# Kernel optimization log

Measured on AMD Instinct MI355X. Metric: run time of the kernel, lower is better.

Reference implementation:

```python
import jax, jax.numpy as jnp
import numpy as np

N_EXPERTS = 8
D_IN = 2048
D_OUT = 2048
BATCH = 8192


def setup_inputs() -> dict:
    key = jax.random.key(0)
    k_x, k_w, k_b, k_a, k_m = jax.random.split(key, 5)
    xs = jax.random.normal(k_x, (BATCH, D_IN), dtype=jnp.float32)
    # Expert parameters: each submodule modeled as Linear(D_IN, D_OUT)
    W = jax.random.normal(k_w, (N_EXPERTS, D_IN, D_OUT), dtype=jnp.float32) / np.sqrt(D_IN)
    b = jax.random.normal(k_b, (N_EXPERTS, D_OUT), dtype=jnp.float32) * 0.01
    actions = jax.random.randint(k_a, (BATCH,), 0, N_EXPERTS, dtype=jnp.int32)
    mxs = jax.random.randint(k_m, (BATCH,), 0, N_EXPERTS, dtype=jnp.int32)  # pass-through metadata
    return {"xs": xs, "W": W, "b": b, "mxs": mxs, "actions": actions}


def reference(xs, W, b, mxs, actions):
    # Original: per-sample split, route sample i to submodule actions[i], concat.
    # Vectorized MoE dispatch-combine: compute all expert outputs, select by one-hot.
    onehot = jax.nn.one_hot(actions, W.shape[0], dtype=xs.dtype)  # [B, E]
    # y_all[b,e,f] = xs[b,:] @ W[e,:,:]; combine with one-hot selection, add routed bias.
    ys = jnp.einsum('be,bd,edf->bf', onehot, xs, W) + b[actions]  # [B, D_OUT]
    return (ys, mxs, actions)
```

## Files before the change

kernel.cpp:

```cpp
#include <hip/hip_runtime.h>
#include <hip/hip_bf16.h>
#include <stdint.h>

#define BATCH 8192
#define BATCH_PAD (BATCH + 128)
#define DIN   2048
#define DOUT  2048
#define NEXP  8
#define BM    128
#define BN    256
#define BK    64
#define NT    (DIN / BK)
#define ASZ   16384
#define TSZ   49152

typedef __attribute__((ext_vector_type(4))) float fx4;
typedef __attribute__((ext_vector_type(8))) short sx8;

__device__ __forceinline__ short f2b(float x){
  unsigned u = __float_as_uint(x);
  u = u + 0x7FFFu + ((u >> 16) & 1u);
  return (short)(u >> 16);
}

__device__ __forceinline__ void gload16(const void* g, void* l){
  __builtin_amdgcn_global_load_lds(
      (const __attribute__((address_space(1))) unsigned int*)g,
      (__attribute__((address_space(3))) unsigned int*)l, 16, 0, 0);
}

__global__ void prep_kernel(const int* __restrict__ actions, const int* __restrict__ mxs,
                            int* __restrict__ perm, int* __restrict__ cnt_off,
                            float* __restrict__ out){
  __shared__ int cnt[NEXP], off[NEXP], cur[NEXP];
  int t = threadIdx.x;
  if (t < NEXP) cnt[t] = 0;
  __syncthreads();
  for (int i = t; i < BATCH; i += 256){
    atomicAdd(&cnt[actions[i]], 1);
    out[(size_t)BATCH * DOUT + i]         = (float)mxs[i];
    out[(size_t)BATCH * DOUT + BATCH + i] = (float)actions[i];
  }
  __syncthreads();
  if (t == 0){ int s = 0; for (int e = 0; e < NEXP; ++e){ off[e] = s; cur[e] = s; s += cnt[e]; } }
  __syncthreads();
  for (int i = t; i < BATCH; i += 256){
    int e = actions[i];
    int p = atomicAdd(&cur[e], 1);
    perm[p] = i;
  }
  if (t < NEXP){ cnt_off[t] = cnt[t]; cnt_off[NEXP + t] = off[t]; }
}

__global__ void gatherx_kernel(const float* __restrict__ xs, const int* __restrict__ perm,
                               short* __restrict__ xp){
  int i = blockIdx.x;
  int t = threadIdx.x;
  short v[8];
  if (i < BATCH){
    const fx4* src = (const fx4*)(xs + (size_t)perm[i] * DIN + t * 8);
    fx4 a = src[0], b2 = src[1];
    v[0]=f2b(a.x); v[1]=f2b(a.y); v[2]=f2b(a.z); v[3]=f2b(a.w);
    v[4]=f2b(b2.x); v[5]=f2b(b2.y); v[6]=f2b(b2.z); v[7]=f2b(b2.w);
  } else {
#pragma unroll
    for (int j = 0; j < 8; ++j) v[j] = 0;
  }
  *(sx8*)(xp + (size_t)i * DIN + t * 8) = *(const sx8*)v;
}

__global__ void transw_kernel(const float* __restrict__ W, short* __restrict__ Wt){
  __shared__ float tile[64][69];
  int e  = blockIdx.z;
  int n0 = blockIdx.x * 64;
  int k0 = blockIdx.y * 64;
  const float* Wp = W + (size_t)e * DIN * DOUT + (size_t)k0 * DOUT + n0;
  int t = threadIdx.x;
#pragma unroll
  for (int it = 0; it < 4; ++it){
    int r = it * 16 + (t >> 4);
    int c = (t & 15) * 4;
    fx4 v = *(const fx4*)(Wp + (size_t)r * DOUT + c);
    tile[r][c] = v.x; tile[r][c+1] = v.y; tile[r][c+2] = v.z; tile[r][c+3] = v.w;
  }
  __syncthreads();
  int n  = t >> 2;
  int kc = (t & 3) * 16;
  short vv[16];
#pragma unroll
  for (int j = 0; j < 16; ++j) vv[j] = f2b(tile[kc + j][n]);
  short* dst = Wt + (size_t)e * DOUT * DIN + (size_t)(n0 + n) * DIN + k0 + kc;
  *(sx8*)dst       = *(const sx8*)vv;
  *(sx8*)(dst + 8) = *(const sx8*)(vv + 8);
}

__global__ __launch_bounds__(512, 2)
void moe_gemm_kernel(const short* __restrict__ xp, const short* __restrict__ Wt,
                     const float* __restrict__ bias, const int* __restrict__ perm,
                     const int* __restrict__ cnt_off, float* __restrict__ out){
  extern __shared__ char lds[];

  int F    = blockIdx.x;
  int J    = (F & 7) * 512 + (F >> 3);
  int g    = J >> 6;
  int slot = J & 63;
  int e    = g >> 3;
  int nb   = g & 7;
  int cnt_e = cnt_off[e];
  if (slot * BM >= cnt_e) return;
  int off_e  = cnt_off[NEXP + e];
  int m_base = off_e + slot * BM;
  int m_cnt  = min(BM, cnt_e - slot * BM);
  int n0     = nb * BN;

  int t    = threadIdx.x;
  int wid  = t >> 6;
  int l    = t & 63;
  int wm   = wid & 1;
  int wn   = wid >> 1;
  int lrow = l & 15;
  int lk   = l >> 4;

  int csrc = (((t & 7) ^ ((t >> 3) & 7)) << 4);
  const char* agp[2];
  const char* bgp[4];
  {
    const char* xpB = (const char*)xp;
    const char* wtB = (const char*)Wt + (size_t)e * ((size_t)DOUT * DIN * 2);
#pragma unroll
    for (int j = 0; j < 2; ++j){
      int r = j * 64 + (t >> 3);
      agp[j] = xpB + (size_t)(m_base + r) * (DIN * 2) + csrc;
    }
#pragma unroll
    for (int j = 0; j < 4; ++j){
      int r = j * 64 + (t >> 3);
      bgp[j] = wtB + (size_t)(n0 + r) * (DIN * 2) + csrc;
    }
  }
  int da0 = t * 16,        da1 = 8192  + t * 16;
  int db0 = ASZ + t * 16,  db1 = ASZ + 8192 + t * 16;
  int db2 = ASZ + 16384 + t * 16, db3 = ASZ + 24576 + t * 16;

#define STG1(kt, base) do{ gload16(agp[0] + (size_t)(kt)*128, lds + (base) + da0); \
                           gload16(agp[1] + (size_t)(kt)*128, lds + (base) + da1); \
                           gload16(bgp[0] + (size_t)(kt)*128, lds + (base) + db0);}while(0)
#define STG2(kt, base) do{ gload16(bgp[1] + (size_t)(kt)*128, lds + (base) + db1); \
                           gload16(bgp[2] + (size_t)(kt)*128, lds + (base) + db2); \
                           gload16(bgp[3] + (size_t)(kt)*128, lds + (base) + db3);}while(0)

  int sw = (lrow & 7) << 4;
  int aoff[2][4], boff[2][4];
#pragma unroll
  for (int kk = 0; kk < 2; ++kk){
#pragma unroll
    for (int m = 0; m < 4; ++m)
      aoff[kk][m] = (wm * 64 + m * 16 + lrow) * 128 + (((kk * 4 + lk) * 16) ^ sw);
#pragma unroll
    for (int n = 0; n < 4; ++n)
      boff[kk][n] = ASZ + (wn * 64 + n * 16 + lrow) * 128 + (((kk * 4 + lk) * 16) ^ sw);
  }

  fx4 acc[4][4];
#pragma unroll
  for (int m = 0; m < 4; ++m)
#pragma unroll
    for (int n = 0; n < 4; ++n)
      acc[m][n] = (fx4){0.f, 0.f, 0.f, 0.f};

  float bcol[4];
#pragma unroll
  for (int n = 0; n < 4; ++n)
    bcol[n] = bias[(size_t)e * DOUT + n0 + wn * 64 + n * 16 + lrow];

  STG1(0, 0);     STG2(0, 0);
  STG1(1, TSZ);   STG2(1, TSZ);
  asm volatile("s_waitcnt vmcnt(6)" ::: "memory");
  __builtin_amdgcn_s_barrier();
  asm volatile("" ::: "memory");

  sx8 a0[4], a1[4], b0[4], b1[4];
#pragma unroll
  for (int m = 0; m < 4; ++m) a0[m] = *(const sx8*)(lds + aoff[0][m]);
#pragma unroll
  for (int n = 0; n < 4; ++n) b0[n] = *(const sx8*)(lds + boff[0][n]);

  int cmp = 0, nxt = TSZ, stg = 2 * TSZ;

  for (int kt = 0; kt < NT; ++kt){
#pragma unroll
    for (int m = 0; m < 4; ++m) a1[m] = *(const sx8*)(lds + cmp + aoff[1][m]);
#pragma unroll
    for (int n = 0; n < 4; ++n) b1[n] = *(const sx8*)(lds + cmp + boff[1][n]);
    if (kt + 2 < NT) STG1(kt + 2, stg);
    __builtin_amdgcn_s_setprio(1);
#pragma unroll
    for (int m = 0; m < 4; ++m)
#pragma unroll
      for (int n = 0; n < 4; ++n)
        acc[m][n] = __builtin_amdgcn_mfma_f32_16x16x32_bf16(a0[m], b0[n], acc[m][n], 0, 0, 0);
    __builtin_amdgcn_s_setprio(0);
    __builtin_amdgcn_s_barrier();
    asm volatile("" ::: "memory");

    if (kt + 2 < NT){
      STG2(kt + 2, stg);
      asm volatile("s_waitcnt vmcnt(6)" ::: "memory");
    } else {
      asm volatile("s_waitcnt vmcnt(0)" ::: "memory");
    }
    __builtin_amdgcn_s_barrier();
    asm volatile("" ::: "memory");
    if (kt + 1 < NT){
#pragma unroll
      for (int m = 0; m < 4; ++m) a0[m] = *(const sx8*)(lds + nxt + aoff[0][m]);
#pragma unroll
      for (int n = 0; n < 4; ++n) b0[n] = *(const sx8*)(lds + nxt + boff[0][n]);
    }
    __builtin_amdgcn_s_setprio(1);
#pragma unroll
    for (int m = 0; m < 4; ++m)
#pragma unroll
      for (int n = 0; n < 4; ++n)
        acc[m][n] = __builtin_amdgcn_mfma_f32_16x16x32_bf16(a1[m], b1[n], acc[m][n], 0, 0, 0);
    __builtin_amdgcn_s_setprio(0);
    __builtin_amdgcn_s_barrier();
    asm volatile("" ::: "memory");

    int tmp = cmp; cmp = nxt; nxt = stg; stg = tmp;
  }

#pragma unroll
  for (int m = 0; m < 4; ++m){
    int rb = wm * 64 + m * 16 + lk * 4;
    int prow[4];
#pragma unroll
    for (int q = 0; q < 4; ++q)
      prow[q] = (rb + q < m_cnt) ? perm[m_base + rb + q] : -1;
#pragma unroll
    for (int n = 0; n < 4; ++n){
      int col = n0 + wn * 64 + n * 16 + lrow;
      fx4 v = acc[m][n];
#pragma unroll
      for (int q = 0; q < 4; ++q)
        if (prow[q] >= 0)
          out[(size_t)prow[q] * DOUT + col] = v[q] + bcol[n];
    }
  }
#undef STG1
#undef STG2
}

extern "C" void kernel_launch(void* const* d_in, const int* in_sizes, int n_in,
                              void* d_out, int out_size, void* d_ws, size_t ws_size,
                              hipStream_t stream) {
  const float* xs      = (const float*)d_in[0];
  const float* W       = (const float*)d_in[1];
  const float* b       = (const float*)d_in[2];
  const int*   mxs     = (const int*)d_in[3];
  const int*   actions = (const int*)d_in[4];
  float* out = (float*)d_out;

  int*   perm    = (int*)d_ws;
  int*   cnt_off = perm + BATCH;
  short* Wt      = (short*)((char*)d_ws + 65536);
  short* xp      = (short*)((char*)d_ws + 65536 + (size_t)NEXP * DIN * DOUT * 2);

  hipLaunchKernelGGL(prep_kernel, dim3(1), dim3(256), 0, stream, actions, mxs, perm, cnt_off, out);
  hipLaunchKernelGGL(gatherx_kernel, dim3(BATCH_PAD), dim3(256), 0, stream, xs, perm, xp);
  hipLaunchKernelGGL(transw_kernel, dim3(DOUT/64, DIN/64, NEXP), dim3(256), 0, stream, W, Wt);
  hipLaunchKernelGGL(moe_gemm_kernel, dim3(64 * 64), dim3(512), 147456, stream,
                     xp, Wt, b, perm, cnt_off, out);
}
```

Baseline: 187.5 us.

## Pad expert groups to tile multiples, compact grid, halve BK with triple-buffered LDS

Expert row groups are now padded to multiples of 128 in the permutation, and a compact slot-to-expert table replaces the sparse 4096-block grid with about 576 blocks. The GEMM K tile drops from 64 to 32, giving a triple-buffered 72KB static LDS footprint and launch bounds raised to four blocks per CU. It also uses a new swizzled LDS layout and a single-phase k-step. This removes empty-block launch overhead and aims for higher occupancy, at the cost of more barriers per K and some padded rows computed on zeros.

```diff
diff --git a/kernel.cpp b/kernel.cpp
--- a/kernel.cpp
+++ b/kernel.cpp
@@ -3,16 +3,17 @@
 #include <stdint.h>
 
 #define BATCH 8192
-#define BATCH_PAD (BATCH + 128)
+#define GROWS 9216
 #define DIN   2048
 #define DOUT  2048
 #define NEXP  8
 #define BM    128
 #define BN    256
-#define BK    64
+#define BK    32
 #define NT    (DIN / BK)
-#define ASZ   16384
-#define TSZ   49152
+#define NSLOT 72
+#define BUFSZ 24576
+#define BOFF  8192
 
 typedef __attribute__((ext_vector_type(4))) float fx4;
 typedef __attribute__((ext_vector_type(8))) short sx8;
@@ -30,10 +31,11 @@
 }
 
 __global__ void prep_kernel(const int* __restrict__ actions, const int* __restrict__ mxs,
-                            int* __restrict__ perm, int* __restrict__ cnt_off,
+                            int* __restrict__ perm, int* __restrict__ meta,
                             float* __restrict__ out){
-  __shared__ int cnt[NEXP], off[NEXP], cur[NEXP];
+  __shared__ int cnt[NEXP], cur[NEXP];
   int t = threadIdx.x;
+  for (int i = t; i < GROWS; i += 256) perm[i] = -1;
   if (t < NEXP) cnt[t] = 0;
   __syncthreads();
   for (int i = t; i < BATCH; i += 256){
@@ -42,14 +44,21 @@
     out[(size_t)BATCH * DOUT + BATCH + i] = (float)actions[i];
   }
   __syncthreads();
-  if (t == 0){ int s = 0; for (int e = 0; e < NEXP; ++e){ off[e] = s; cur[e] = s; s += cnt[e]; } }
+  if (t == 0){
+    int s = 0, slot = 0;
+    for (int e = 0; e < NEXP; ++e){
+      cur[e] = s;
+      int ns = (cnt[e] + BM - 1) / BM;
+      for (int q = 0; q < ns; ++q) meta[17 + slot++] = e;
+      s += ns * BM;
+    }
+    meta[16] = slot;
+  }
   __syncthreads();
   for (int i = t; i < BATCH; i += 256){
     int e = actions[i];
-    int p = atomicAdd(&cur[e], 1);
-    perm[p] = i;
-  }
-  if (t < NEXP){ cnt_off[t] = cnt[t]; cnt_off[NEXP + t] = off[t]; }
+    perm[atomicAdd(&cur[e], 1)] = i;
+  }
 }
 
 __global__ void gatherx_kernel(const float* __restrict__ xs, const int* __restrict__ perm,
@@ -57,8 +66,9 @@
   int i = blockIdx.x;
   int t = threadIdx.x;
   short v[8];
-  if (i < BATCH){
-    const fx4* src = (const fx4*)(xs + (size_t)perm[i] * DIN + t * 8);
+  int p = perm[i];
+  if (p >= 0){
+    const fx4* src = (const fx4*)(xs + (size_t)p * DIN + t * 8);
     fx4 a = src[0], b2 = src[1];
     v[0]=f2b(a.x); v[1]=f2b(a.y); v[2]=f2b(a.z); v[3]=f2b(a.w);
     v[4]=f2b(b2.x); v[5]=f2b(b2.y); v[6]=f2b(b2.z); v[7]=f2b(b2.w);
@@ -94,23 +104,18 @@
   *(sx8*)(dst + 8) = *(const sx8*)(vv + 8);
 }
 
-__global__ __launch_bounds__(512, 2)
+__global__ __launch_bounds__(512, 4)
 void moe_gemm_kernel(const short* __restrict__ xp, const short* __restrict__ Wt,
                      const float* __restrict__ bias, const int* __restrict__ perm,
-                     const int* __restrict__ cnt_off, float* __restrict__ out){
-  extern __shared__ char lds[];
-
-  int F    = blockIdx.x;
-  int J    = (F & 7) * 512 + (F >> 3);
-  int g    = J >> 6;
-  int slot = J & 63;
-  int e    = g >> 3;
-  int nb   = g & 7;
-  int cnt_e = cnt_off[e];
-  if (slot * BM >= cnt_e) return;
-  int off_e  = cnt_off[NEXP + e];
-  int m_base = off_e + slot * BM;
-  int m_cnt  = min(BM, cnt_e - slot * BM);
+                     const int* __restrict__ meta, float* __restrict__ out){
+  __shared__ char lds[3 * BUFSZ];
+
+  int F = blockIdx.x;
+  int slot = F >> 3, nb = F & 7;
+  int nslots = meta[16];
+  if (slot >= nslots) return;
+  int e      = meta[17 + slot];
+  int m_base = slot * BM;
   int n0     = nb * BN;
 
   int t    = threadIdx.x;
@@ -121,45 +126,25 @@
   int lrow = l & 15;
   int lk   = l >> 4;
 
-  int csrc = (((t & 7) ^ ((t >> 3) & 7)) << 4);
-  const char* agp[2];
-  const char* bgp[4];
-  {
-    const char* xpB = (const char*)xp;
-    const char* wtB = (const char*)Wt + (size_t)e * ((size_t)DOUT * DIN * 2);
-#pragma unroll
-    for (int j = 0; j < 2; ++j){
-      int r = j * 64 + (t >> 3);
-      agp[j] = xpB + (size_t)(m_base + r) * (DIN * 2) + csrc;
-    }
-#pragma unroll
-    for (int j = 0; j < 4; ++j){
-      int r = j * 64 + (t >> 3);
-      bgp[j] = wtB + (size_t)(n0 + r) * (DIN * 2) + csrc;
-    }
-  }
-  int da0 = t * 16,        da1 = 8192  + t * 16;
-  int db0 = ASZ + t * 16,  db1 = ASZ + 8192 + t * 16;
-  int db2 = ASZ + 16384 + t * 16, db3 = ASZ + 24576 + t * 16;
-
-#define STG1(kt, base) do{ gload16(agp[0] + (size_t)(kt)*128, lds + (base) + da0); \
-                           gload16(agp[1] + (size_t)(kt)*128, lds + (base) + da1); \
-                           gload16(bgp[0] + (size_t)(kt)*128, lds + (base) + db0);}while(0)
-#define STG2(kt, base) do{ gload16(bgp[1] + (size_t)(kt)*128, lds + (base) + db1); \
-                           gload16(bgp[2] + (size_t)(kt)*128, lds + (base) + db2); \
-                           gload16(bgp[3] + (size_t)(kt)*128, lds + (base) + db3);}while(0)
-
-  int sw = (lrow & 7) << 4;
-  int aoff[2][4], boff[2][4];
-#pragma unroll
-  for (int kk = 0; kk < 2; ++kk){
-#pragma unroll
-    for (int m = 0; m < 4; ++m)
-      aoff[kk][m] = (wm * 64 + m * 16 + lrow) * 128 + (((kk * 4 + lk) * 16) ^ sw);
-#pragma unroll
-    for (int n = 0; n < 4; ++n)
-      boff[kk][n] = ASZ + (wn * 64 + n * 16 + lrow) * 128 + (((kk * 4 + lk) * 16) ^ sw);
-  }
+  int srow = ((t >> 3) << 1) | ((t >> 2) & 1);
+  int schk = (t & 3) ^ ((t >> 3) & 3);
+  const char* ag  = (const char*)xp + ((size_t)(m_base + srow) * DIN + schk * 8) * 2;
+  const char* bg0 = (const char*)Wt + (((size_t)e * DOUT + n0 + srow) * DIN + schk * 8) * 2;
+  const char* bg1 = bg0 + (size_t)128 * DIN * 2;
+  int ldst = t * 16;
+
+#define STAGE(kt, BASE) do{ \
+    gload16(ag  + (size_t)(kt) * 64, lds + (BASE) + ldst); \
+    gload16(bg0 + (size_t)(kt) * 64, lds + (BASE) + BOFF + ldst); \
+    gload16(bg1 + (size_t)(kt) * 64, lds + (BASE) + BOFF + 8192 + ldst); \
+  }while(0)
+
+  int arow = wm * 64 + lrow;
+  int aline = arow >> 1;
+  int addrA = aline * 128 + (arow & 1) * 64 + ((lk ^ (aline & 3)) << 4);
+  int brow = wn * 64 + lrow;
+  int bline = brow >> 1;
+  int addrB = BOFF + bline * 128 + (brow & 1) * 64 + ((lk ^ (bline & 3)) << 4);
 
   fx4 acc[4][4];
 #pragma unroll
@@ -173,62 +158,39 @@
   for (int n = 0; n < 4; ++n)
     bcol[n] = bias[(size_t)e * DOUT + n0 + wn * 64 + n * 16 + lrow];
 
-  STG1(0, 0);     STG2(0, 0);
-  STG1(1, TSZ);   STG2(1, TSZ);
-  asm volatile("s_waitcnt vmcnt(6)" ::: "memory");
+#define KSTEP(CB, SB, DOSTG, kt) do{ \
+    sx8 af[4], bf[4]; \
+    _Pragma("unroll") for (int m = 0; m < 4; ++m) \
+      af[m] = *(const sx8*)(lds + (CB) + addrA + m * 1024); \
+    _Pragma("unroll") for (int n = 0; n < 4; ++n) \
+      bf[n] = *(const sx8*)(lds + (CB) + addrB + n * 1024); \
+    if (DOSTG) STAGE((kt) + 2, SB); \
+    __builtin_amdgcn_s_setprio(1); \
+    _Pragma("unroll") for (int m = 0; m < 4; ++m) \
+    _Pragma("unroll") for (int n = 0; n < 4; ++n) \
+      acc[m][n] = __builtin_amdgcn_mfma_f32_16x16x32_bf16(af[m], bf[n], acc[m][n], 0, 0, 0); \
+    __builtin_amdgcn_s_setprio(0); \
+    if (DOSTG) asm volatile("s_waitcnt vmcnt(3)" ::: "memory"); \
+    else       asm volatile("s_waitcnt vmcnt(0)" ::: "memory"); \
+    __builtin_amdgcn_s_barrier(); \
+    asm volatile("" ::: "memory"); \
+  }while(0)
+
+  STAGE(0, 0);
+  STAGE(1, BUFSZ);
+  asm volatile("s_waitcnt vmcnt(3)" ::: "memory");
   __builtin_amdgcn_s_barrier();
   asm volatile("" ::: "memory");
 
-  sx8 a0[4], a1[4], b0[4], b1[4];
-#pragma unroll
-  for (int m = 0; m < 4; ++m) a0[m] = *(const sx8*)(lds + aoff[0][m]);
-#pragma unroll
-  for (int n = 0; n < 4; ++n) b0[n] = *(const sx8*)(lds + boff[0][n]);
-
-  int cmp = 0, nxt = TSZ, stg = 2 * TSZ;
-
-  for (int kt = 0; kt < NT; ++kt){
-#pragma unroll
-    for (int m = 0; m < 4; ++m) a1[m] = *(const sx8*)(lds + cmp + aoff[1][m]);
-#pragma unroll
-    for (int n = 0; n < 4; ++n) b1[n] = *(const sx8*)(lds + cmp + boff[1][n]);
-    if (kt + 2 < NT) STG1(kt + 2, stg);
-    __builtin_amdgcn_s_setprio(1);
-#pragma unroll
-    for (int m = 0; m < 4; ++m)
-#pragma unroll
-      for (int n = 0; n < 4; ++n)
-        acc[m][n] = __builtin_amdgcn_mfma_f32_16x16x32_bf16(a0[m], b0[n], acc[m][n], 0, 0, 0);
-    __builtin_amdgcn_s_setprio(0);
-    __builtin_amdgcn_s_barrier();
-    asm volatile("" ::: "memory");
-
-    if (kt + 2 < NT){
-      STG2(kt + 2, stg);
-      asm volatile("s_waitcnt vmcnt(6)" ::: "memory");
-    } else {
-      asm volatile("s_waitcnt vmcnt(0)" ::: "memory");
-    }
-    __builtin_amdgcn_s_barrier();
-    asm volatile("" ::: "memory");
-    if (kt + 1 < NT){
-#pragma unroll
-      for (int m = 0; m < 4; ++m) a0[m] = *(const sx8*)(lds + nxt + aoff[0][m]);
-#pragma unroll
-      for (int n = 0; n < 4; ++n) b0[n] = *(const sx8*)(lds + nxt + boff[0][n]);
-    }
-    __builtin_amdgcn_s_setprio(1);
-#pragma unroll
-    for (int m = 0; m < 4; ++m)
-#pragma unroll
-      for (int n = 0; n < 4; ++n)
-        acc[m][n] = __builtin_amdgcn_mfma_f32_16x16x32_bf16(a1[m], b1[n], acc[m][n], 0, 0, 0);
-    __builtin_amdgcn_s_setprio(0);
-    __builtin_amdgcn_s_barrier();
-    asm volatile("" ::: "memory");
-
-    int tmp = cmp; cmp = nxt; nxt = stg; stg = tmp;
-  }
+  for (int kt = 0; kt < 60; kt += 3){
+    KSTEP(0,         2*BUFSZ, 1, kt);
+    KSTEP(BUFSZ,     0,       1, kt + 1);
+    KSTEP(2*BUFSZ,   BUFSZ,   1, kt + 2);
+  }
+  KSTEP(0,       2*BUFSZ, 1, 60);
+  KSTEP(BUFSZ,   0,       1, 61);
+  KSTEP(2*BUFSZ, 0,       0, 62);
+  KSTEP(0,       0,       0, 63);
 
 #pragma unroll
   for (int m = 0; m < 4; ++m){
@@ -236,7 +198,7 @@
     int prow[4];
 #pragma unroll
     for (int q = 0; q < 4; ++q)
-      prow[q] = (rb + q < m_cnt) ? perm[m_base + rb + q] : -1;
+      prow[q] = perm[m_base + rb + q];
 #pragma unroll
     for (int n = 0; n < 4; ++n){
       int col = n0 + wn * 64 + n * 16 + lrow;
@@ -247,8 +209,8 @@
           out[(size_t)prow[q] * DOUT + col] = v[q] + bcol[n];
     }
   }
-#undef STG1
-#undef STG2
+#undef KSTEP
+#undef STAGE
 }
 
 extern "C" void kernel_launch(void* const* d_in, const int* in_sizes, int n_in,
@@ -261,14 +223,14 @@
   const int*   actions = (const int*)d_in[4];
   float* out = (float*)d_out;
 
-  int*   perm    = (int*)d_ws;
-  int*   cnt_off = perm + BATCH;
-  short* Wt      = (short*)((char*)d_ws + 65536);
-  short* xp      = (short*)((char*)d_ws + 65536 + (size_t)NEXP * DIN * DOUT * 2);
-
-  hipLaunchKernelGGL(prep_kernel, dim3(1), dim3(256), 0, stream, actions, mxs, perm, cnt_off, out);
-  hipLaunchKernelGGL(gatherx_kernel, dim3(BATCH_PAD), dim3(256), 0, stream, xs, perm, xp);
+  int*   perm = (int*)d_ws;
+  int*   meta = (int*)((char*)d_ws + 40960);
+  short* Wt   = (short*)((char*)d_ws + 65536);
+  short* xp   = (short*)((char*)d_ws + 65536 + (size_t)NEXP * DIN * DOUT * 2);
+
+  hipLaunchKernelGGL(prep_kernel, dim3(1), dim3(256), 0, stream, actions, mxs, perm, meta, out);
+  hipLaunchKernelGGL(gatherx_kernel, dim3(GROWS), dim3(256), 0, stream, xs, perm, xp);
   hipLaunchKernelGGL(transw_kernel, dim3(DOUT/64, DIN/64, NEXP), dim3(256), 0, stream, W, Wt);
-  hipLaunchKernelGGL(moe_gemm_kernel, dim3(64 * 64), dim3(512), 147456, stream,
-                     xp, Wt, b, perm, cnt_off, out);
-}
+  hipLaunchKernelGGL(moe_gemm_kernel, dim3(NSLOT * 8), dim3(512), 0, stream,
+                     xp, Wt, b, perm, meta, out);
+}
```

Result: no change. 190.5 us (+1.6%).
